# Performance work log

Hardware: AMD Instinct MI355X
Metric: run time of the kernel (lower is better)

The kernel has to match this reference:

```python
import jax, jax.numpy as jnp
import numpy as np

B, C, H, W = 32, 64, 56, 56
REPN, NK, SMALL = 50, 17, 3   # repN=64-int(64*0.23), nk=ceil(51/3)
GROUPS = 4                     # N_rep
EPS = 1e-5


def _build_index_mats():
    """Reduce the fallback's python scatter-add loops to exact linear maps.
    For flat position p=r*NK+j the roll shifts depend only on p%3, so each
    shift class s gets a (REPN,NK) count matrix over source nk-slots."""
    rng = np.random.RandomState(123)
    ghost = np.sort(rng.choice(C, C - REPN, replace=False))
    rep = np.array(sorted(set(range(C)) - set(ghost.tolist())), np.int32)
    Mh = np.zeros((3, REPN, NK), np.int32)
    Mv = np.zeros((3, REPN, NK), np.int32)
    Mid = np.zeros((REPN, NK), np.int32)
    for _ in range(GROUPS):
        for r in range(REPN):
            perm = rng.permutation(NK)
            for p in range(NK):
                Mh[(r * NK + p) % 3, r, perm[p]] += 1
        for r in range(REPN):
            perm = rng.permutation(NK)
            for p in range(NK):
                Mv[(r * NK + p) % 3, r, perm[p]] += 1
        kk = rng.randint(0, NK, REPN)
        for r in range(REPN):
            Mid[r, kk[r]] += 1
    return ghost.astype(np.int32), rep, Mh, Mv, Mid


def setup_inputs() -> dict:
    key = jax.random.key(0)
    k1, k2, k3 = jax.random.split(key, 3)
    ghost, rep, Mh, Mv, Mid = _build_index_mats()
    return {
        "inputs": jax.random.normal(k1, (B, C, H, W), jnp.float32),
        "w0": jax.random.normal(k2, (REPN * NK, 1, SMALL, SMALL), jnp.float32) * 0.1,
        "w1": jax.random.normal(k3, (REPN * NK, 1, SMALL, SMALL), jnp.float32) * 0.1,
        "Mh": jnp.asarray(Mh), "Mv": jnp.asarray(Mv), "Mid": jnp.asarray(Mid),
        "ghost_idx": jnp.asarray(ghost), "rep_idx": jnp.asarray(rep),
    }


def _bn(x):
    # BatchNorm2d in training mode, affine weight=1 / bias=0 (init values)
    m = x.mean(axis=(0, 2, 3), keepdims=True)
    v = x.var(axis=(0, 2, 3), keepdims=True)
    return (x - m) / jnp.sqrt(v + EPS)


def reference(inputs, w0, w1, Mh, Mv, Mid, ghost_idx, rep_idx):
    rep_in = inputs[:, rep_idx]      # (B, REPN, H, W)
    ghost_in = inputs[:, ghost_idx]  # (B, ghostN, H, W)

    def conv(w):  # depthwise-grouped conv: groups=REPN, each 1->NK channels
        return jax.lax.conv_general_dilated(
            rep_in, w, window_strides=(1, 1), padding=((2, 2), (2, 2)),
            dimension_numbers=('NCHW', 'OIHW', 'NCHW'),
            feature_group_count=REPN)

    out = conv(w0) + conv(w1)                       # (B, REPN*NK, H+2, W+2)
    xv = out.reshape(B, REPN, NK, H + 2, W + 2)

    Mhf, Mvf, Midf = (m.astype(xv.dtype) for m in (Mh, Mv, Mid))
    sh1, sw1 = (0, 1, 2), (0, 2, 1)   # lora1: shifts (i%3, 2i%3)
    sh2, sw2 = (0, 2, 1), (0, 1, 2)   # lora2: shifts (2i%3, i%3)

    lora1 = sum(jnp.roll(jnp.einsum('rk,brkhw->brhw', Mhf[s], xv),
                         (sh1[s], sw1[s]), axis=(2, 3)) for s in range(3))
    lora2 = sum(jnp.roll(jnp.einsum('rk,brkhw->brhw', Mvf[s], xv),
                         (sh2[s], sw2[s]), axis=(2, 3)) for s in range(3))
    small = jnp.einsum('rk,brkhw->brhw', Midf, xv)

    # center-crop back to (H, W): dh = dw = 1
    lora1 = lora1[:, :, 1:1 + H, 1:1 + W]
    lora2 = lora2[:, :, 1:1 + H, 1:1 + W]
    small = small[:, :, 1:1 + H, 1:1 + W]

    x = _bn(lora1) + _bn(lora2) + _bn(small) + rep_in
    return jnp.concatenate([x, ghost_in], axis=1)   # (B, C, H, W)
```

## Files before the change

### kernel.cpp

```cpp
#include <hip/hip_runtime.h>

#define Bn 32
#define Cn 64
#define Hn 56
#define Wn 56
#define REPN 50
#define NKn 17
#define HWn (Hn*Wn)
#define NSTATf 100352.0f
#define EPSf 1e-5f

#define TSTR 64
#define TROWS 60
#define TSZ (TROWS*TSTR)

#define WEFF_OFF 0
#define STATS_OFF 3200

__global__ void k_weff(const float* __restrict__ w0, const float* __restrict__ w1,
                       const int* __restrict__ Mh, const int* __restrict__ Mv,
                       const int* __restrict__ Mid, float* __restrict__ ws)
{
    int idx = blockIdx.x * blockDim.x + threadIdx.x;
    if (idx < 6*REPN) ws[STATS_OFF + idx] = 0.f;
    if (idx >= REPN*63) return;
    int r   = idx / 63;
    int rem = idx % 63;
    int t   = rem / 9;
    int ij  = rem % 9;
    const int* M = (t < 3) ? (Mh + (t*REPN + r)*NKn)
                 : (t < 6) ? (Mv + ((t-3)*REPN + r)*NKn)
                           : (Mid + r*NKn);
    float acc = 0.f;
    for (int k = 0; k < NKn; ++k) {
        int m = M[k];
        if (m) acc += (float)m * (w0[(r*NKn + k)*9 + ij] + w1[(r*NKn + k)*9 + ij]);
    }
    ws[WEFF_OFF + idx] = acc;
}

__device__ __forceinline__ float dot9(const float n[9], const float* __restrict__ wk) {
    return n[0]*wk[0] + n[1]*wk[1] + n[2]*wk[2]
         + n[3]*wk[3] + n[4]*wk[4] + n[5]*wk[5]
         + n[6]*wk[6] + n[7]*wk[7] + n[8]*wk[8];
}

__device__ __forceinline__ void load9(const float* __restrict__ tile, int y, int x, float n[9]) {
    const float* b = tile + y*TSTR + x + 2;
    n[0] = b[0];        n[1] = b[1];        n[2] = b[2];
    n[3] = b[TSTR];     n[4] = b[TSTR+1];   n[5] = b[TSTR+2];
    n[6] = b[2*TSTR];   n[7] = b[2*TSTR+1]; n[8] = b[2*TSTR+2];
}

__device__ __forceinline__ void compute3(const float* __restrict__ tile,
                                         const float* __restrict__ wk,
                                         int h, int w,
                                         float& l1, float& l2, float& sm)
{
    float n[9];
    load9(tile, h + 1, w + 1, n);
    l1 = dot9(n, wk + 0);
    l2 = dot9(n, wk + 27);
    sm = dot9(n, wk + 54);
    int xa = (w == 0) ? 57 : (w - 1);
    load9(tile, h, xa, n);
    l1 += dot9(n, wk + 9);
    l2 += dot9(n, wk + 45);
    int yb = (h == 0) ? 57 : (h - 1);
    load9(tile, yb, w, n);
    l1 += dot9(n, wk + 18);
    l2 += dot9(n, wk + 36);
}

__device__ __forceinline__ void load_tile(const float* __restrict__ src,
                                          float* __restrict__ tile, int tid)
{
    for (int i = tid; i < TSZ; i += 256) tile[i] = 0.f;
    __syncthreads();
    const float4* s4 = (const float4*)src;
    for (int i = tid; i < HWn/4; i += 256) {
        float4 v = s4[i];
        int e = i * 4;
        int row = e / Wn;
        int col = e % Wn;
        *(float4*)(tile + (2 + row)*TSTR + 4 + col) = v;
    }
    __syncthreads();
}

__global__ void __launch_bounds__(256) k_stats(const float* __restrict__ in,
        const int* __restrict__ rep_idx, const float* __restrict__ weff,
        float* __restrict__ stats)
{
    __shared__ __align__(16) float tile[TSZ];
    __shared__ float red[4][6];
    int bid = blockIdx.x;
    int r = bid % REPN;
    int b = bid / REPN;
    int tid = threadIdx.x;
    int cin = rep_idx[r];
    load_tile(in + ((size_t)(b*Cn + cin))*HWn, tile, tid);

    float wk[63];
    const float* wr = weff + r*63;
    #pragma unroll
    for (int i = 0; i < 63; ++i) wk[i] = wr[i];

    float s1=0.f,q1=0.f,s2=0.f,q2=0.f,s3=0.f,q3=0.f;
    for (int p = tid; p < HWn; p += 256) {
        int h = p / Wn, w = p % Wn;
        float l1, l2, sm;
        compute3(tile, wk, h, w, l1, l2, sm);
        s1 += l1; q1 += l1*l1;
        s2 += l2; q2 += l2*l2;
        s3 += sm; q3 += sm*sm;
    }
    float vals[6] = {s1,q1,s2,q2,s3,q3};
    int lane = tid & 63, wave = tid >> 6;
    #pragma unroll
    for (int q = 0; q < 6; ++q) {
        float v = vals[q];
        for (int o = 32; o; o >>= 1) v += __shfl_down(v, o, 64);
        if (lane == 0) red[wave][q] = v;
    }
    __syncthreads();
    if (tid < 6)
        atomicAdd(&stats[tid*REPN + r], red[0][tid] + red[1][tid] + red[2][tid] + red[3][tid]);
}

__global__ void __launch_bounds__(256) k_out(const float* __restrict__ in,
        const int* __restrict__ rep_idx, const int* __restrict__ ghost_idx,
        const float* __restrict__ weff, const float* __restrict__ stats,
        float* __restrict__ out)
{
    __shared__ __align__(16) float tile[TSZ];
    int bid = blockIdx.x;
    int c = bid % Cn;
    int b = bid / Cn;
    int tid = threadIdx.x;

    if (c >= REPN) {
        int cin = ghost_idx[c - REPN];
        const float4* s4 = (const float4*)(in + ((size_t)(b*Cn + cin))*HWn);
        float4* d4 = (float4*)(out + ((size_t)(b*Cn + c))*HWn);
        for (int i = tid; i < HWn/4; i += 256) d4[i] = s4[i];
        return;
    }

    int r = c;
    int cin = rep_idx[r];
    load_tile(in + ((size_t)(b*Cn + cin))*HWn, tile, tid);

    float wk[63];
    const float* wr = weff + r*63;
    #pragma unroll
    for (int i = 0; i < 63; ++i) wk[i] = wr[i];

    const float inv = 1.0f / NSTATf;
    float m1 = stats[0*REPN+r]*inv, v1 = stats[1*REPN+r]*inv - m1*m1;
    float m2 = stats[2*REPN+r]*inv, v2 = stats[3*REPN+r]*inv - m2*m2;
    float m3 = stats[4*REPN+r]*inv, v3 = stats[5*REPN+r]*inv - m3*m3;
    float r1 = rsqrtf(v1 + EPSf), r2 = rsqrtf(v2 + EPSf), r3 = rsqrtf(v3 + EPSf);

    float* dst = out + ((size_t)(b*Cn + c))*HWn;
    for (int p = tid; p < HWn; p += 256) {
        int h = p / Wn, w = p % Wn;
        float l1, l2, sm;
        compute3(tile, wk, h, w, l1, l2, sm);
        dst[p] = (l1 - m1)*r1 + (l2 - m2)*r2 + (sm - m3)*r3 + tile[(2 + h)*TSTR + 4 + w];
    }
}

extern "C" void kernel_launch(void* const* d_in, const int* in_sizes, int n_in,
                              void* d_out, int out_size, void* d_ws, size_t ws_size,
                              hipStream_t stream) {
    const float* in   = (const float*)d_in[0];
    const float* w0   = (const float*)d_in[1];
    const float* w1   = (const float*)d_in[2];
    const int*   Mh   = (const int*)d_in[3];
    const int*   Mv   = (const int*)d_in[4];
    const int*   Mid  = (const int*)d_in[5];
    const int*   ghost= (const int*)d_in[6];
    const int*   rep  = (const int*)d_in[7];
    float* out  = (float*)d_out;
    float* ws   = (float*)d_ws;
    float* weff  = ws + WEFF_OFF;
    float* stats = ws + STATS_OFF;

    k_weff<<<(REPN*63 + 255)/256, 256, 0, stream>>>(w0, w1, Mh, Mv, Mid, ws);
    k_stats<<<Bn*REPN, 256, 0, stream>>>(in, rep, weff, stats);
    k_out<<<Bn*Cn, 256, 0, stream>>>(in, rep, ghost, weff, stats, out);
}
```

Before: 140.8 us.

## Compute four adjacent outputs per thread with vectorized LDS row loads

Replaces the per-pixel 27-load stencil with a per-thread quad of four horizontal outputs. Each thread loads a few tile rows as float4 pairs and reuses them across all three shifted 3x3 windows. The tile stride becomes 68, which changes LDS bank mapping and keeps the row reads 16-byte aligned. Outputs are written as float4 and the zero-fill is vectorized. This cuts LDS traffic and address arithmetic, at the cost of more registers per thread and intricate wrap-around edge handling (top row and left column) that could introduce correctness errors.

```diff
diff --git a/kernel.cpp b/kernel.cpp
--- a/kernel.cpp
+++ b/kernel.cpp
@@ -10,12 +10,14 @@
 #define NSTATf 100352.0f
 #define EPSf 1e-5f
 
-#define TSTR 64
+#define TSTR 68
 #define TROWS 60
 #define TSZ (TROWS*TSTR)
 
 #define WEFF_OFF 0
 #define STATS_OFF 3200
+
+#define NQ 784
 
 __global__ void k_weff(const float* __restrict__ w0, const float* __restrict__ w1,
                        const int* __restrict__ Mh, const int* __restrict__ Mv,
@@ -39,43 +41,10 @@
     ws[WEFF_OFF + idx] = acc;
 }
 
-__device__ __forceinline__ float dot9(const float n[9], const float* __restrict__ wk) {
-    return n[0]*wk[0] + n[1]*wk[1] + n[2]*wk[2]
-         + n[3]*wk[3] + n[4]*wk[4] + n[5]*wk[5]
-         + n[6]*wk[6] + n[7]*wk[7] + n[8]*wk[8];
-}
-
-__device__ __forceinline__ void load9(const float* __restrict__ tile, int y, int x, float n[9]) {
-    const float* b = tile + y*TSTR + x + 2;
-    n[0] = b[0];        n[1] = b[1];        n[2] = b[2];
-    n[3] = b[TSTR];     n[4] = b[TSTR+1];   n[5] = b[TSTR+2];
-    n[6] = b[2*TSTR];   n[7] = b[2*TSTR+1]; n[8] = b[2*TSTR+2];
-}
-
-__device__ __forceinline__ void compute3(const float* __restrict__ tile,
-                                         const float* __restrict__ wk,
-                                         int h, int w,
-                                         float& l1, float& l2, float& sm)
-{
-    float n[9];
-    load9(tile, h + 1, w + 1, n);
-    l1 = dot9(n, wk + 0);
-    l2 = dot9(n, wk + 27);
-    sm = dot9(n, wk + 54);
-    int xa = (w == 0) ? 57 : (w - 1);
-    load9(tile, h, xa, n);
-    l1 += dot9(n, wk + 9);
-    l2 += dot9(n, wk + 45);
-    int yb = (h == 0) ? 57 : (h - 1);
-    load9(tile, yb, w, n);
-    l1 += dot9(n, wk + 18);
-    l2 += dot9(n, wk + 36);
-}
-
 __device__ __forceinline__ void load_tile(const float* __restrict__ src,
                                           float* __restrict__ tile, int tid)
 {
-    for (int i = tid; i < TSZ; i += 256) tile[i] = 0.f;
+    for (int i = tid; i < TSZ/4; i += 256) *(float4*)(tile + 4*i) = make_float4(0,0,0,0);
     __syncthreads();
     const float4* s4 = (const float4*)src;
     for (int i = tid; i < HWn/4; i += 256) {
@@ -88,6 +57,83 @@
     __syncthreads();
 }
 
+__device__ __forceinline__ void conv_quad(const float* __restrict__ tile,
+        const float* __restrict__ wk, int g,
+        float* __restrict__ l1, float* __restrict__ l2,
+        float* __restrict__ sm, float* __restrict__ res)
+{
+    int h  = g / 14;
+    int wq = g - h*14;
+    int w0 = wq * 4;
+    bool topwrap = (h == 0);
+    #pragma unroll
+    for (int p = 0; p < 4; ++p) { l1[p]=0.f; l2[p]=0.f; sm[p]=0.f; }
+
+    {
+        int row = topwrap ? 57 : (h-1);
+        const float* rp = tile + row*TSTR + w0;
+        float4 qa = *(const float4*)rp;
+        float4 qb = *(const float4*)(rp+4);
+        float X[8] = {qa.x,qa.y,qa.z,qa.w,qb.x,qb.y,qb.z,qb.w};
+        #pragma unroll
+        for (int p = 0; p < 4; ++p)
+            #pragma unroll
+            for (int j = 0; j < 3; ++j) {
+                float v = X[2+p+j];
+                l1[p] = fmaf(v, wk[18+j], l1[p]);
+                l2[p] = fmaf(v, wk[36+j], l2[p]);
+            }
+    }
+    #pragma unroll
+    for (int d = 0; d < 4; ++d) {
+        const float* rp = tile + (h+d)*TSTR + w0;
+        float4 qa = *(const float4*)rp;
+        float4 qb = *(const float4*)(rp+4);
+        float X[9] = {qa.x,qa.y,qa.z,qa.w,qb.x,qb.y,qb.z,qb.w,0.f};
+        if (d >= 1) X[8] = rp[8];
+        if (d == 2) { res[0]=X[4]; res[1]=X[5]; res[2]=X[6]; res[3]=X[7]; }
+        if (d <= 1) {
+            #pragma unroll
+            for (int p = 0; p < 4; ++p)
+                #pragma unroll
+                for (int j = 0; j < 3; ++j) {
+                    float v = topwrap ? 0.f : X[2+p+j];
+                    l1[p] = fmaf(v, wk[21+3*d+j], l1[p]);
+                    l2[p] = fmaf(v, wk[39+3*d+j], l2[p]);
+                }
+        }
+        if (d <= 2) {
+            #pragma unroll
+            for (int p = 0; p < 4; ++p)
+                #pragma unroll
+                for (int j = 0; j < 3; ++j) {
+                    float v = X[1+p+j];
+                    l1[p] = fmaf(v, wk[9+3*d+j],  l1[p]);
+                    l2[p] = fmaf(v, wk[45+3*d+j], l2[p]);
+                }
+        }
+        if (d >= 1) {
+            #pragma unroll
+            for (int p = 0; p < 4; ++p)
+                #pragma unroll
+                for (int j = 0; j < 3; ++j) {
+                    float v = X[3+p+j];
+                    l1[p] = fmaf(v, wk[3*(d-1)+j],    l1[p]);
+                    l2[p] = fmaf(v, wk[27+3*(d-1)+j], l2[p]);
+                    sm[p] = fmaf(v, wk[54+3*(d-1)+j], sm[p]);
+                }
+        }
+    }
+    if (wq == 0) {
+        #pragma unroll
+        for (int d = 0; d < 3; ++d) {
+            float v = tile[(h+d)*TSTR + 59];
+            l1[0] = fmaf(v, wk[9+3*d],  l1[0]);
+            l2[0] = fmaf(v, wk[45+3*d], l2[0]);
+        }
+    }
+}
+
 __global__ void __launch_bounds__(256) k_stats(const float* __restrict__ in,
         const int* __restrict__ rep_idx, const float* __restrict__ weff,
         float* __restrict__ stats)
@@ -107,13 +153,15 @@
     for (int i = 0; i < 63; ++i) wk[i] = wr[i];
 
     float s1=0.f,q1=0.f,s2=0.f,q2=0.f,s3=0.f,q3=0.f;
-    for (int p = tid; p < HWn; p += 256) {
-        int h = p / Wn, w = p % Wn;
-        float l1, l2, sm;
-        compute3(tile, wk, h, w, l1, l2, sm);
-        s1 += l1; q1 += l1*l1;
-        s2 += l2; q2 += l2*l2;
-        s3 += sm; q3 += sm*sm;
+    for (int g = tid; g < NQ; g += 256) {
+        float l1[4], l2[4], sm[4], res[4];
+        conv_quad(tile, wk, g, l1, l2, sm, res);
+        #pragma unroll
+        for (int p = 0; p < 4; ++p) {
+            s1 += l1[p]; q1 += l1[p]*l1[p];
+            s2 += l2[p]; q2 += l2[p]*l2[p];
+            s3 += sm[p]; q3 += sm[p]*sm[p];
+        }
     }
     float vals[6] = {s1,q1,s2,q2,s3,q3};
     int lane = tid & 63, wave = tid >> 6;
@@ -163,11 +211,17 @@
     float r1 = rsqrtf(v1 + EPSf), r2 = rsqrtf(v2 + EPSf), r3 = rsqrtf(v3 + EPSf);
 
     float* dst = out + ((size_t)(b*Cn + c))*HWn;
-    for (int p = tid; p < HWn; p += 256) {
-        int h = p / Wn, w = p % Wn;
-        float l1, l2, sm;
-        compute3(tile, wk, h, w, l1, l2, sm);
-        dst[p] = (l1 - m1)*r1 + (l2 - m2)*r2 + (sm - m3)*r3 + tile[(2 + h)*TSTR + 4 + w];
+    for (int g = tid; g < NQ; g += 256) {
+        float l1[4], l2[4], sm[4], res[4];
+        conv_quad(tile, wk, g, l1, l2, sm, res);
+        int h  = g / 14;
+        int w0 = (g - h*14) * 4;
+        float4 o;
+        o.x = (l1[0]-m1)*r1 + (l2[0]-m2)*r2 + (sm[0]-m3)*r3 + res[0];
+        o.y = (l1[1]-m1)*r1 + (l2[1]-m2)*r2 + (sm[1]-m3)*r3 + res[1];
+        o.z = (l1[2]-m1)*r1 + (l2[2]-m2)*r2 + (sm[2]-m3)*r3 + res[2];
+        o.w = (l1[3]-m1)*r1 + (l2[3]-m2)*r2 + (sm[3]-m3)*r3 + res[3];
+        *(float4*)(dst + h*Wn + w0) = o;
     }
 }
 
```

Result: slower. 149.3 us (+6.0%).
